# Optimization experiments

Measured on AMD Instinct MI355X. Metric: run time of the kernel, lower is better.

Reference implementation:

```python
import jax, jax.numpy as jnp
import numpy as np

EMBED_DIM = 512
NUM_HEADS = 8
HEAD_DIM = EMBED_DIM // NUM_HEADS
PAIR_BONUS = 2.0
MIN_SEPARATION = 3
PAIRING_MATRIX = jnp.array([
    [0, 1, 0, 0, 0],
    [1, 0, 1, 0, 0],
    [0, 1, 0, 1, 0],
    [0, 0, 1, 0, 0],
    [0, 0, 0, 0, 0],
], dtype=jnp.float32)


def setup_inputs() -> dict:
    key = jax.random.key(0)
    ks = jax.random.split(key, 12)
    B, S, E = 8, 1024, EMBED_DIM
    scale = 1.0 / np.sqrt(E)
    inp = {
        "query": jax.random.normal(ks[0], (B, S, E), dtype=jnp.float32),
        "key": jax.random.normal(ks[1], (B, S, E), dtype=jnp.float32),
        "value": jax.random.normal(ks[2], (B, S, E), dtype=jnp.float32),
        "nucleotide_sequence": jax.random.randint(ks[3], (B, S), 0, 5, dtype=jnp.int32),
        "key_padding_mask": jnp.zeros((B, S), dtype=bool),
        "Wq": jax.random.normal(ks[4], (E, E), dtype=jnp.float32) * scale,
        "bq": jnp.zeros((E,), dtype=jnp.float32),
        "Wk": jax.random.normal(ks[5], (E, E), dtype=jnp.float32) * scale,
        "bk": jnp.zeros((E,), dtype=jnp.float32),
        "Wv": jax.random.normal(ks[6], (E, E), dtype=jnp.float32) * scale,
        "bv": jnp.zeros((E,), dtype=jnp.float32),
        "Wo": jax.random.normal(ks[7], (E, E), dtype=jnp.float32) * scale,
        "bo": jnp.zeros((E,), dtype=jnp.float32),
    }
    return inp


def reference(query, key, value, nucleotide_sequence, key_padding_mask,
              Wq, bq, Wk, bk, Wv, bv, Wo, bo):
    B, T, E = query.shape
    S = key.shape[1]
    H, D = NUM_HEADS, HEAD_DIM
    scaling = D ** -0.5

    # projections -> (B, H, L, D)
    q = (query @ Wq + bq).reshape(B, T, H, D).transpose(0, 2, 1, 3)
    k = (key @ Wk + bk).reshape(B, S, H, D).transpose(0, 2, 1, 3)
    v = (value @ Wv + bv).reshape(B, S, H, D).transpose(0, 2, 1, 3)

    attn = jnp.einsum('bhtd,bhsd->bhts', q, k) * scaling  # (B,H,T,S)

    # base-pairing bias: gather into 5x5 table, masked by min separation
    pos = jnp.arange(S)
    sep_ok = (jnp.abs(pos[:, None] - pos[None, :]) >= MIN_SEPARATION).astype(jnp.float32)
    pairing = PAIRING_MATRIX[nucleotide_sequence[:, :, None], nucleotide_sequence[:, None, :]]  # (B,S,S)
    pair_bonus = pairing * sep_ok[None] * PAIR_BONUS
    attn = attn + pair_bonus[:, None, :, :]

    # key padding mask -> -inf
    attn = jnp.where(key_padding_mask[:, None, None, :], -jnp.inf, attn)

    attn_probs = jax.nn.softmax(attn, axis=-1)
    out = jnp.einsum('bhts,bhsd->bhtd', attn_probs, v)
    out = out.transpose(0, 2, 1, 3).reshape(B, T, E)
    out = out @ Wo + bo
    return out, attn_probs
```

## Files before the change

kernel.cpp:

```cpp
#include <hip/hip_runtime.h>
#include <hip/hip_bf16.h>
#include <stdint.h>


typedef float  f32x4  __attribute__((ext_vector_type(4)));
typedef short  s16x8  __attribute__((ext_vector_type(8)));

__device__ __forceinline__ ushort f2bf(float f) {
  union { float f; uint32_t u; } v; v.f = f;
  uint32_t u = v.u;
  return (ushort)((u + 0x7FFF + ((u >> 16) & 1)) >> 16);
}

__device__ __forceinline__ f32x4 mfma16(s16x8 a, s16x8 b, f32x4 c) {
  return __builtin_amdgcn_mfma_f32_16x16x32_bf16(a, b, c, 0, 0, 0);
}

__device__ __forceinline__ void gl_lds16(const void* g, void* l) {
  typedef __attribute__((address_space(1))) const void gvoid;
  typedef __attribute__((address_space(3))) void lvoid;
  __builtin_amdgcn_global_load_lds((gvoid*)(uintptr_t)g,
                                   (lvoid*)(uint32_t)(uintptr_t)l, 16, 0, 0);
}

__global__ __launch_bounds__(256) void k_convert_qkv(
    const float* __restrict__ q, const float* __restrict__ k,
    const float* __restrict__ v, ushort* __restrict__ Xbf) {
  size_t i = (size_t)blockIdx.x * 256 + threadIdx.x;
#pragma unroll
  for (int it = 0; it < 3; it++) {
    const float* src = (it == 0) ? q : (it == 1 ? k : v);
    float4 x = *reinterpret_cast<const float4*>(&src[i * 4]);
    uint2 o;
    o.x = (uint32_t)f2bf(x.x) | ((uint32_t)f2bf(x.y) << 16);
    o.y = (uint32_t)f2bf(x.z) | ((uint32_t)f2bf(x.w) << 16);
    *reinterpret_cast<uint2*>(&Xbf[((size_t)it * 1048576 + i) * 4]) = o;
  }
}

__global__ __launch_bounds__(256) void k_convert_w(
    const float* __restrict__ Wq, const float* __restrict__ Wk,
    const float* __restrict__ Wv, const float* __restrict__ Wo,
    ushort* __restrict__ WT, ushort* __restrict__ WoT) {
  int idx = blockIdx.x * 256 + threadIdx.x;
  int row = idx >> 9;
  int k = idx & 511;
  if (row < 1536) {
    const float* W = (row < 512) ? Wq : (row < 1024 ? Wk : Wv);
    int n = row & 511;
    WT[row * 512 + k] = f2bf(W[k * 512 + n]);
  } else {
    int n = row - 1536;
    WoT[n * 512 + k] = f2bf(Wo[k * 512 + n]);
  }
}

__global__ __launch_bounds__(256) void k_gemm_qkv(
    const ushort* __restrict__ Xbf, const ushort* __restrict__ WT,
    const float* __restrict__ bq, const float* __restrict__ bk,
    const float* __restrict__ bv, ushort* __restrict__ Y) {
  __shared__ ushort As[128 * 64];
  __shared__ ushort Bs[128 * 64];
  const int id = blockIdx.x;
  const int xcd = id & 7, slot = id >> 3;
  const int mb = xcd * 8 + slot / 12;
  const int nb = slot % 12;
  const int mat = nb >> 2;
  const float* bias = (mat == 0) ? bq : (mat == 1 ? bk : bv);
  const ushort* A = Xbf + (size_t)mat * 8192 * 512;
  const int tid = threadIdx.x;
  const int w = tid >> 6, l = tid & 63;
  const int wr = (w >> 1) * 64, wc = (w & 1) * 64;
  const int lr = l & 15, lg = l >> 4;
  const int srow = l >> 3, sslot = (l & 7) ^ srow;

  f32x4 acc[4][4];
#pragma unroll
  for (int i = 0; i < 4; i++)
#pragma unroll
    for (int j = 0; j < 4; j++) acc[i][j] = (f32x4){0.f, 0.f, 0.f, 0.f};

  for (int kk = 0; kk < 8; kk++) {
    const int k0 = kk * 64;
#pragma unroll
    for (int it = 0; it < 4; it++) {
      int g8 = it * 4 + w;
      int row = g8 * 8 + srow;
      gl_lds16(&A[(size_t)(mb * 128 + row) * 512 + k0 + sslot * 8], &As[g8 * 512]);
      gl_lds16(&WT[(size_t)(nb * 128 + row) * 512 + k0 + sslot * 8], &Bs[g8 * 512]);
    }
    __syncthreads();
#pragma unroll
    for (int ks = 0; ks < 2; ks++) {
      s16x8 af[4], bfr[4];
#pragma unroll
      for (int mt = 0; mt < 4; mt++) {
        int row = wr + mt * 16 + lr;
        af[mt] = *reinterpret_cast<const s16x8*>(
            (char*)As + row * 128 + ((ks * 64 + lg * 16) ^ ((row & 7) << 4)));
      }
#pragma unroll
      for (int nt = 0; nt < 4; nt++) {
        int row = wc + nt * 16 + lr;
        bfr[nt] = *reinterpret_cast<const s16x8*>(
            (char*)Bs + row * 128 + ((ks * 64 + lg * 16) ^ ((row & 7) << 4)));
      }
#pragma unroll
      for (int mt = 0; mt < 4; mt++)
#pragma unroll
        for (int nt = 0; nt < 4; nt++)
          acc[mt][nt] = mfma16(af[mt], bfr[nt], acc[mt][nt]);
    }
    __syncthreads();
  }
  const int ncb = nb * 128;
#pragma unroll
  for (int nt = 0; nt < 4; nt++) {
    int gcol = ncb + wc + nt * 16 + lr;
    float bv_ = bias[gcol & 511];
#pragma unroll
    for (int mt = 0; mt < 4; mt++) {
#pragma unroll
      for (int r = 0; r < 4; r++) {
        int grow = mb * 128 + wr + mt * 16 + lg * 4 + r;
        Y[(size_t)grow * 1536 + gcol] = f2bf(acc[mt][nt][r] + bv_);
      }
    }
  }
}

__global__ __launch_bounds__(256) void k_transpose_v(
    const ushort* __restrict__ Y, ushort* __restrict__ vT) {
  __shared__ ushort T[64 * 64];
  const int sc = blockIdx.x;
  const int bh = blockIdx.y;
  const int b = bh >> 3, h = bh & 7;
  const int s0 = sc * 64;
  const int tid = threadIdx.x;
#pragma unroll
  for (int it = 0; it < 2; it++) {
    int slot = it * 256 + tid;
    int srw = slot >> 3;
    int i16 = (slot & 7) * 16;
    int4 v = *reinterpret_cast<const int4*>(
        &Y[(size_t)(b * 1024 + s0 + srw) * 1536 + 1024 + h * 64 + (slot & 7) * 8]);
    *reinterpret_cast<int4*>((char*)T + srw * 128 + (i16 ^ ((srw & 7) << 4))) = v;
  }
  __syncthreads();
  const int d = tid >> 2;
  const int sseg = (tid & 3) * 16;
  int pk[8];
#pragma unroll
  for (int j = 0; j < 8; j++) {
    int s0l = sseg + 2 * j;
    uint32_t a = *reinterpret_cast<const ushort*>(
        (char*)T + s0l * 128 + ((d * 2) ^ ((s0l & 7) << 4)));
    uint32_t bb = *reinterpret_cast<const ushort*>(
        (char*)T + (s0l + 1) * 128 + ((d * 2) ^ (((s0l + 1) & 7) << 4)));
    pk[j] = (int)(a | (bb << 16));
  }
  ushort* dst = &vT[(size_t)(bh * 64 + d) * 1024 + s0 + sseg];
  int4 o0 = {pk[0], pk[1], pk[2], pk[3]};
  int4 o1 = {pk[4], pk[5], pk[6], pk[7]};
  *reinterpret_cast<int4*>(dst) = o0;
  *reinterpret_cast<int4*>(dst + 8) = o1;
}

__global__ __launch_bounds__(256) void k_attention(
    const ushort* __restrict__ Y, const ushort* __restrict__ vT,
    const int* __restrict__ seq, const unsigned char* __restrict__ mask,
    float* __restrict__ probs, ushort* __restrict__ AO) {
  __shared__ ushort Kb[2][64 * 64];
  __shared__ float Pb[16 * 68];
  __shared__ int seqm[1024];
  __shared__ float Rbuf[4 * 4 * 4 * 16];
  __shared__ float rinv_s[16];

  const int id = blockIdx.x;
  const int xcd = id & 7, slot = id >> 3;
  const int bh = xcd * 8 + (slot >> 6);
  const int tb = slot & 63;
  const int b = bh >> 3, h = bh & 7;
  const int tid = threadIdx.x;
  const int w = tid >> 6, l = tid & 63;
  const int lr = l & 15, lg = l >> 4;
  const int sc_ = w * 16;
  const int srow = l >> 3, sslot = (l & 7) ^ srow;

#pragma unroll
  for (int it = 0; it < 4; it++) {
    int s = it * 256 + tid;
    seqm[s] = seq[b * 1024 + s] | (mask[b * 1024 + s] ? 0x100 : 0);
  }
  const ushort* qp = &Y[(size_t)(b * 1024 + tb * 16 + lr) * 1536 + h * 64 + lg * 8];
  s16x8 qf0 = *reinterpret_cast<const s16x8*>(qp);
  s16x8 qf1 = *reinterpret_cast<const s16x8*>(qp + 32);

  f32x4 e[16];
  float psum[4] = {0.f, 0.f, 0.f, 0.f};

#pragma unroll
  for (int it = 0; it < 2; it++) {
    int g8 = it * 4 + w;
    int row = g8 * 8 + srow;
    gl_lds16(&Y[(size_t)(b * 1024 + row) * 1536 + 512 + h * 64 + sslot * 8],
             &Kb[0][g8 * 512]);
  }
  __syncthreads();

  int seqt[4];
#pragma unroll
  for (int r = 0; r < 4; r++) seqt[r] = seqm[tb * 16 + lg * 4 + r] & 255;

#pragma unroll
  for (int c = 0; c < 16; c++) {
    if (c < 15) {
#pragma unroll
      for (int it = 0; it < 2; it++) {
        int g8 = it * 4 + w;
        int row = (c + 1) * 64 + g8 * 8 + srow;
        gl_lds16(&Y[(size_t)(b * 1024 + row) * 1536 + 512 + h * 64 + sslot * 8],
                 &Kb[(c + 1) & 1][g8 * 512]);
      }
    }
    f32x4 facc = (f32x4){0.f, 0.f, 0.f, 0.f};
    const int srw = sc_ + lr;
#pragma unroll
    for (int ks = 0; ks < 2; ks++) {
      s16x8 kf = *reinterpret_cast<const s16x8*>(
          (char*)&Kb[c & 1][0] + srw * 128 + ((ks * 64 + lg * 16) ^ ((srw & 7) << 4)));
      facc = mfma16(ks == 0 ? qf0 : qf1, kf, facc);
    }
    const int sg = c * 64 + srw;
    const int sm = seqm[sg];
    const int ss = sm & 255;
    const bool msk = (sm & 0x100) != 0;
    f32x4 ev;
#pragma unroll
    for (int r = 0; r < 4; r++) {
      int tg = tb * 16 + lg * 4 + r;
      int dsep = tg - sg; dsep = dsep < 0 ? -dsep : dsep;
      int dnt = seqt[r] - ss; dnt = dnt < 0 ? -dnt : dnt;
      float bonus = (dnt == 1 && seqt[r] <= 3 && ss <= 3 && dsep >= 3) ? 2.0f : 0.0f;
      float v = facc[r] * 0.125f + bonus;
      float ee = msk ? 0.0f : __expf(v - 12.0f);
      ev[r] = ee;
      psum[r] += ee;
    }
    e[c] = ev;
    __syncthreads();
  }

#pragma unroll
  for (int r = 0; r < 4; r++) Rbuf[((w * 4 + lg) * 4 + r) * 16 + lr] = psum[r];
  __syncthreads();
  {
    int row = tid >> 4, j = tid & 15;
    int lgr = row >> 2, rr = row & 3;
    float s = 0.f;
#pragma unroll
    for (int i = 0; i < 4; i++) {
      int wj = j >> 2;
      int lrj = (j & 3) * 4 + i;
      s += Rbuf[((wj * 4 + lgr) * 4 + rr) * 16 + lrj];
    }
#pragma unroll
    for (int off = 1; off < 16; off <<= 1) s += __shfl_xor(s, off);
    if (j == 0) rinv_s[row] = 1.0f / s;
  }
  __syncthreads();
#pragma unroll
  for (int it = 0; it < 2; it++) {
    int g8 = it * 4 + w;
    int d = g8 * 8 + srow;
    gl_lds16(&vT[(size_t)(bh * 64 + d) * 1024 + sslot * 8], &Kb[0][g8 * 512]);
  }

  float rv[4];
#pragma unroll
  for (int r = 0; r < 4; r++) rv[r] = rinv_s[lg * 4 + r];
  const float rvp = rinv_s[tid >> 4];

  f32x4 oacc = (f32x4){0.f, 0.f, 0.f, 0.f};
#pragma unroll
  for (int c = 0; c < 16; c++) {
#pragma unroll
    for (int r = 0; r < 4; r++) Pb[(lg * 4 + r) * 68 + sc_ + lr] = e[c][r];
    __syncthreads();
    if (c < 15) {
#pragma unroll
      for (int it = 0; it < 2; it++) {
        int g8 = it * 4 + w;
        int d = g8 * 8 + srow;
        gl_lds16(&vT[(size_t)(bh * 64 + d) * 1024 + (c + 1) * 64 + sslot * 8],
                 &Kb[(c + 1) & 1][g8 * 512]);
      }
    }
#pragma unroll
    for (int ks = 0; ks < 2; ks++) {
      const float* pp = &Pb[lr * 68 + ks * 32 + lg * 8];
      float4 pa = *reinterpret_cast<const float4*>(pp);
      float4 pb = *reinterpret_cast<const float4*>(pp + 4);
      s16x8 paf = {(short)f2bf(pa.x), (short)f2bf(pa.y), (short)f2bf(pa.z),
                   (short)f2bf(pa.w), (short)f2bf(pb.x), (short)f2bf(pb.y),
                   (short)f2bf(pb.z), (short)f2bf(pb.w)};
      const int drow = sc_ + lr;
      s16x8 vb = *reinterpret_cast<const s16x8*>(
          (char*)&Kb[c & 1][0] + drow * 128 + ((ks * 64 + lg * 16) ^ ((drow & 7) << 4)));
      oacc = mfma16(paf, vb, oacc);
    }
    {
      int row = tid >> 4, j = tid & 15;
      float4 p4 = *reinterpret_cast<const float4*>(&Pb[row * 68 + j * 4]);
      float4 o;
      o.x = p4.x * rvp; o.y = p4.y * rvp; o.z = p4.z * rvp; o.w = p4.w * rvp;
      *reinterpret_cast<float4*>(
          &probs[((size_t)bh * 1024 + tb * 16 + row) * 1024 + c * 64 + j * 4]) = o;
    }
    __syncthreads();
  }
#pragma unroll
  for (int r = 0; r < 4; r++) {
    int t = tb * 16 + lg * 4 + r;
    AO[((size_t)b * 1024 + t) * 512 + h * 64 + sc_ + lr] = f2bf(oacc[r] * rv[r]);
  }
}

__global__ __launch_bounds__(256) void k_gemm_o(
    const ushort* __restrict__ AO, const ushort* __restrict__ WoT,
    const float* __restrict__ bo, float* __restrict__ out) {
  __shared__ ushort As[128 * 64];
  __shared__ ushort Bs[128 * 64];
  const int id = blockIdx.x;
  const int xcd = id & 7, slot = id >> 3;
  const int mb = xcd * 8 + (slot >> 2);
  const int nb = slot & 3;
  const int tid = threadIdx.x;
  const int w = tid >> 6, l = tid & 63;
  const int wr = (w >> 1) * 64, wc = (w & 1) * 64;
  const int lr = l & 15, lg = l >> 4;
  const int srow = l >> 3, sslot = (l & 7) ^ srow;

  f32x4 acc[4][4];
#pragma unroll
  for (int i = 0; i < 4; i++)
#pragma unroll
    for (int j = 0; j < 4; j++) acc[i][j] = (f32x4){0.f, 0.f, 0.f, 0.f};

  for (int kk = 0; kk < 8; kk++) {
    const int k0 = kk * 64;
#pragma unroll
    for (int it = 0; it < 4; it++) {
      int g8 = it * 4 + w;
      int row = g8 * 8 + srow;
      gl_lds16(&AO[(size_t)(mb * 128 + row) * 512 + k0 + sslot * 8], &As[g8 * 512]);
      gl_lds16(&WoT[(size_t)(nb * 128 + row) * 512 + k0 + sslot * 8], &Bs[g8 * 512]);
    }
    __syncthreads();
#pragma unroll
    for (int ks = 0; ks < 2; ks++) {
      s16x8 af[4], bfr[4];
#pragma unroll
      for (int mt = 0; mt < 4; mt++) {
        int row = wr + mt * 16 + lr;
        af[mt] = *reinterpret_cast<const s16x8*>(
            (char*)As + row * 128 + ((ks * 64 + lg * 16) ^ ((row & 7) << 4)));
      }
#pragma unroll
      for (int nt = 0; nt < 4; nt++) {
        int row = wc + nt * 16 + lr;
        bfr[nt] = *reinterpret_cast<const s16x8*>(
            (char*)Bs + row * 128 + ((ks * 64 + lg * 16) ^ ((row & 7) << 4)));
      }
#pragma unroll
      for (int mt = 0; mt < 4; mt++)
#pragma unroll
        for (int nt = 0; nt < 4; nt++)
          acc[mt][nt] = mfma16(af[mt], bfr[nt], acc[mt][nt]);
    }
    __syncthreads();
  }
  const int ncb = nb * 128;
#pragma unroll
  for (int nt = 0; nt < 4; nt++) {
    int gcol = ncb + wc + nt * 16 + lr;
    float bv_ = bo[gcol];
#pragma unroll
    for (int mt = 0; mt < 4; mt++) {
#pragma unroll
      for (int r = 0; r < 4; r++) {
        int grow = mb * 128 + wr + mt * 16 + lg * 4 + r;
        out[(size_t)grow * 512 + gcol] = acc[mt][nt][r] + bv_;
      }
    }
  }
}

extern "C" void kernel_launch(void* const* d_in, const int* in_sizes, int n_in,
                              void* d_out, int out_size, void* d_ws, size_t ws_size,
                              hipStream_t stream) {
  (void)in_sizes; (void)n_in; (void)out_size; (void)ws_size;
  const float* query = (const float*)d_in[0];
  const float* key   = (const float*)d_in[1];
  const float* value = (const float*)d_in[2];
  const int* seq     = (const int*)d_in[3];
  const unsigned char* mask = (const unsigned char*)d_in[4];
  const float* Wq = (const float*)d_in[5];
  const float* bq = (const float*)d_in[6];
  const float* Wk = (const float*)d_in[7];
  const float* bk = (const float*)d_in[8];
  const float* Wv = (const float*)d_in[9];
  const float* bv = (const float*)d_in[10];
  const float* Wo = (const float*)d_in[11];
  const float* bo = (const float*)d_in[12];

  float* out = (float*)d_out;
  float* probs = out + (size_t)8 * 1024 * 512;

  char* ws = (char*)d_ws;
  ushort* Y   = (ushort*)(ws);
  ushort* Xbf = (ushort*)(ws + 25165824);
  ushort* WT  = (ushort*)(ws + 50331648);
  ushort* WoT = (ushort*)(ws + 51904512);
  ushort* vT  = (ushort*)(ws + 25165824);
  ushort* AO  = (ushort*)(ws + 33554432);

  k_convert_qkv<<<4096, 256, 0, stream>>>(query, key, value, Xbf);
  k_convert_w<<<4096, 256, 0, stream>>>(Wq, Wk, Wv, Wo, WT, WoT);
  k_gemm_qkv<<<768, 256, 0, stream>>>(Xbf, WT, bq, bk, bv, Y);
  k_transpose_v<<<dim3(16, 64), 256, 0, stream>>>(Y, vT);
  k_attention<<<4096, 256, 0, stream>>>(Y, vT, seq, mask, probs, AO);
  k_gemm_o<<<256, 256, 0, stream>>>(AO, WoT, bo, out);
}
```

Baseline: 216.4 us.

## Fuse fp32-to-bf16 input conversion into QKV GEMM and recompute scores in attention

Removes the separate activation conversion kernel: the QKV GEMM now loads fp32 inputs, converts them to bf16 in registers and writes them into swizzled LDS. The attention kernel no longer keeps the 16 exp tiles in registers. It recomputes QK^T in a second pass, with the bonus and mask bits packed into bitmasks, and reads K and V fragments straight from global memory instead of staging them through LDS. It also sets a launch bound of 4 blocks per CU and writes bf16 probabilities to a smaller LDS tile. This trades register pressure and one kernel launch for doubled QK MFMA work, uncoalesced scalar stores of probs, and synchronous global loads in the GEMM.

```diff
diff --git a/kernel.cpp b/kernel.cpp
--- a/kernel.cpp
+++ b/kernel.cpp
@@ -21,21 +21,6 @@
   typedef __attribute__((address_space(3))) void lvoid;
   __builtin_amdgcn_global_load_lds((gvoid*)(uintptr_t)g,
                                    (lvoid*)(uint32_t)(uintptr_t)l, 16, 0, 0);
-}
-
-__global__ __launch_bounds__(256) void k_convert_qkv(
-    const float* __restrict__ q, const float* __restrict__ k,
-    const float* __restrict__ v, ushort* __restrict__ Xbf) {
-  size_t i = (size_t)blockIdx.x * 256 + threadIdx.x;
-#pragma unroll
-  for (int it = 0; it < 3; it++) {
-    const float* src = (it == 0) ? q : (it == 1 ? k : v);
-    float4 x = *reinterpret_cast<const float4*>(&src[i * 4]);
-    uint2 o;
-    o.x = (uint32_t)f2bf(x.x) | ((uint32_t)f2bf(x.y) << 16);
-    o.y = (uint32_t)f2bf(x.z) | ((uint32_t)f2bf(x.w) << 16);
-    *reinterpret_cast<uint2*>(&Xbf[((size_t)it * 1048576 + i) * 4]) = o;
-  }
 }
 
 __global__ __launch_bounds__(256) void k_convert_w(
@@ -56,7 +41,8 @@
 }
 
 __global__ __launch_bounds__(256) void k_gemm_qkv(
-    const ushort* __restrict__ Xbf, const ushort* __restrict__ WT,
+    const float* __restrict__ Aq, const float* __restrict__ Ak,
+    const float* __restrict__ Av, const ushort* __restrict__ WT,
     const float* __restrict__ bq, const float* __restrict__ bk,
     const float* __restrict__ bv, ushort* __restrict__ Y) {
   __shared__ ushort As[128 * 64];
@@ -66,8 +52,8 @@
   const int mb = xcd * 8 + slot / 12;
   const int nb = slot % 12;
   const int mat = nb >> 2;
+  const float* A    = (mat == 0) ? Aq : (mat == 1 ? Ak : Av);
   const float* bias = (mat == 0) ? bq : (mat == 1 ? bk : bv);
-  const ushort* A = Xbf + (size_t)mat * 8192 * 512;
   const int tid = threadIdx.x;
   const int w = tid >> 6, l = tid & 63;
   const int wr = (w >> 1) * 64, wc = (w & 1) * 64;
@@ -83,10 +69,21 @@
   for (int kk = 0; kk < 8; kk++) {
     const int k0 = kk * 64;
 #pragma unroll
+    for (int it = 0; it < 8; it++) {
+      int s2 = it * 256 + tid;
+      int row = s2 >> 4;
+      int k4 = (s2 & 15) * 4;
+      float4 v = *reinterpret_cast<const float4*>(
+          &A[(size_t)(mb * 128 + row) * 512 + k0 + k4]);
+      uint64_t p = (uint64_t)f2bf(v.x) | ((uint64_t)f2bf(v.y) << 16) |
+                   ((uint64_t)f2bf(v.z) << 32) | ((uint64_t)f2bf(v.w) << 48);
+      int boff = row * 128 + ((k4 * 2) ^ ((row & 7) << 4));
+      *reinterpret_cast<uint64_t*>((char*)As + boff) = p;
+    }
+#pragma unroll
     for (int it = 0; it < 4; it++) {
       int g8 = it * 4 + w;
       int row = g8 * 8 + srow;
-      gl_lds16(&A[(size_t)(mb * 128 + row) * 512 + k0 + sslot * 8], &As[g8 * 512]);
       gl_lds16(&WT[(size_t)(nb * 128 + row) * 512 + k0 + sslot * 8], &Bs[g8 * 512]);
     }
     __syncthreads();
@@ -166,14 +163,13 @@
   *reinterpret_cast<int4*>(dst + 8) = o1;
 }
 
-__global__ __launch_bounds__(256) void k_attention(
+__global__ __launch_bounds__(256, 4) void k_attention(
     const ushort* __restrict__ Y, const ushort* __restrict__ vT,
     const int* __restrict__ seq, const unsigned char* __restrict__ mask,
     float* __restrict__ probs, ushort* __restrict__ AO) {
-  __shared__ ushort Kb[2][64 * 64];
-  __shared__ float Pb[16 * 68];
   __shared__ int seqm[1024];
-  __shared__ float Rbuf[4 * 4 * 4 * 16];
+  __shared__ ushort Pb[16 * 72];
+  __shared__ float Rbuf[1024];
   __shared__ float rinv_s[16];
 
   const int id = blockIdx.x;
@@ -185,7 +181,6 @@
   const int w = tid >> 6, l = tid & 63;
   const int lr = l & 15, lg = l >> 4;
   const int sc_ = w * 16;
-  const int srow = l >> 3, sslot = (l & 7) ^ srow;
 
 #pragma unroll
   for (int it = 0; it < 4; it++) {
@@ -195,60 +190,43 @@
   const ushort* qp = &Y[(size_t)(b * 1024 + tb * 16 + lr) * 1536 + h * 64 + lg * 8];
   s16x8 qf0 = *reinterpret_cast<const s16x8*>(qp);
   s16x8 qf1 = *reinterpret_cast<const s16x8*>(qp + 32);
-
-  f32x4 e[16];
+  __syncthreads();
+
+  int seqt[4];
+#pragma unroll
+  for (int r = 0; r < 4; r++) seqt[r] = seqm[tb * 16 + lg * 4 + r] & 255;
+
+  const ushort* kbase = &Y[(size_t)(b * 1024) * 1536 + 512 + h * 64];
+  const int srw = sc_ + lr;
+
+  uint32_t bb0 = 0, bb1 = 0, mk = 0;
   float psum[4] = {0.f, 0.f, 0.f, 0.f};
-
-#pragma unroll
-  for (int it = 0; it < 2; it++) {
-    int g8 = it * 4 + w;
-    int row = g8 * 8 + srow;
-    gl_lds16(&Y[(size_t)(b * 1024 + row) * 1536 + 512 + h * 64 + sslot * 8],
-             &Kb[0][g8 * 512]);
-  }
-  __syncthreads();
-
-  int seqt[4];
-#pragma unroll
-  for (int r = 0; r < 4; r++) seqt[r] = seqm[tb * 16 + lg * 4 + r] & 255;
-
 #pragma unroll
   for (int c = 0; c < 16; c++) {
-    if (c < 15) {
-#pragma unroll
-      for (int it = 0; it < 2; it++) {
-        int g8 = it * 4 + w;
-        int row = (c + 1) * 64 + g8 * 8 + srow;
-        gl_lds16(&Y[(size_t)(b * 1024 + row) * 1536 + 512 + h * 64 + sslot * 8],
-                 &Kb[(c + 1) & 1][g8 * 512]);
-      }
-    }
+    const int sg = c * 64 + srw;
+    const ushort* kp = kbase + (size_t)sg * 1536;
+    s16x8 kf0 = *reinterpret_cast<const s16x8*>(kp + lg * 8);
+    s16x8 kf1 = *reinterpret_cast<const s16x8*>(kp + 32 + lg * 8);
     f32x4 facc = (f32x4){0.f, 0.f, 0.f, 0.f};
-    const int srw = sc_ + lr;
-#pragma unroll
-    for (int ks = 0; ks < 2; ks++) {
-      s16x8 kf = *reinterpret_cast<const s16x8*>(
-          (char*)&Kb[c & 1][0] + srw * 128 + ((ks * 64 + lg * 16) ^ ((srw & 7) << 4)));
-      facc = mfma16(ks == 0 ? qf0 : qf1, kf, facc);
-    }
-    const int sg = c * 64 + srw;
+    facc = mfma16(qf0, kf0, facc);
+    facc = mfma16(qf1, kf1, facc);
     const int sm = seqm[sg];
     const int ss = sm & 255;
     const bool msk = (sm & 0x100) != 0;
-    f32x4 ev;
+    uint32_t bits = 0;
 #pragma unroll
     for (int r = 0; r < 4; r++) {
       int tg = tb * 16 + lg * 4 + r;
       int dsep = tg - sg; dsep = dsep < 0 ? -dsep : dsep;
       int dnt = seqt[r] - ss; dnt = dnt < 0 ? -dnt : dnt;
-      float bonus = (dnt == 1 && seqt[r] <= 3 && ss <= 3 && dsep >= 3) ? 2.0f : 0.0f;
-      float v = facc[r] * 0.125f + bonus;
+      bool bon = (dnt == 1 && seqt[r] <= 3 && ss <= 3 && dsep >= 3);
+      float v = facc[r] * 0.125f + (bon ? 2.0f : 0.0f);
       float ee = msk ? 0.0f : __expf(v - 12.0f);
-      ev[r] = ee;
       psum[r] += ee;
-    }
-    e[c] = ev;
-    __syncthreads();
+      bits |= (bon ? 1u : 0u) << r;
+    }
+    if (c < 8) bb0 |= bits << (4 * c); else bb1 |= bits << (4 * (c - 8));
+    mk |= (msk ? 1u : 0u) << c;
   }
 
 #pragma unroll
@@ -269,53 +247,38 @@
     if (j == 0) rinv_s[row] = 1.0f / s;
   }
   __syncthreads();
-#pragma unroll
-  for (int it = 0; it < 2; it++) {
-    int g8 = it * 4 + w;
-    int d = g8 * 8 + srow;
-    gl_lds16(&vT[(size_t)(bh * 64 + d) * 1024 + sslot * 8], &Kb[0][g8 * 512]);
-  }
-
   float rv[4];
 #pragma unroll
   for (int r = 0; r < 4; r++) rv[r] = rinv_s[lg * 4 + r];
-  const float rvp = rinv_s[tid >> 4];
 
   f32x4 oacc = (f32x4){0.f, 0.f, 0.f, 0.f};
+  const ushort* vbase = &vT[(size_t)(bh * 64) * 1024];
 #pragma unroll
   for (int c = 0; c < 16; c++) {
-#pragma unroll
-    for (int r = 0; r < 4; r++) Pb[(lg * 4 + r) * 68 + sc_ + lr] = e[c][r];
-    __syncthreads();
-    if (c < 15) {
-#pragma unroll
-      for (int it = 0; it < 2; it++) {
-        int g8 = it * 4 + w;
-        int d = g8 * 8 + srow;
-        gl_lds16(&vT[(size_t)(bh * 64 + d) * 1024 + (c + 1) * 64 + sslot * 8],
-                 &Kb[(c + 1) & 1][g8 * 512]);
-      }
-    }
+    const int sg = c * 64 + srw;
+    const ushort* kp = kbase + (size_t)sg * 1536;
+    s16x8 kf0 = *reinterpret_cast<const s16x8*>(kp + lg * 8);
+    s16x8 kf1 = *reinterpret_cast<const s16x8*>(kp + 32 + lg * 8);
+    f32x4 facc = (f32x4){0.f, 0.f, 0.f, 0.f};
+    facc = mfma16(qf0, kf0, facc);
+    facc = mfma16(qf1, kf1, facc);
+    const uint32_t bits = ((c < 8) ? (bb0 >> (4 * c)) : (bb1 >> (4 * (c - 8)))) & 15u;
+    const bool msk = (mk >> c) & 1u;
+#pragma unroll
+    for (int r = 0; r < 4; r++) {
+      float v = facc[r] * 0.125f + (((bits >> r) & 1u) ? 2.0f : 0.0f);
+      float ee = msk ? 0.0f : __expf(v - 12.0f);
+      probs[((size_t)bh * 1024 + tb * 16 + lg * 4 + r) * 1024 + c * 64 + srw] =
+          ee * rv[r];
+      Pb[(lg * 4 + r) * 72 + srw] = f2bf(ee);
+    }
+    __syncthreads();
 #pragma unroll
     for (int ks = 0; ks < 2; ks++) {
-      const float* pp = &Pb[lr * 68 + ks * 32 + lg * 8];
-      float4 pa = *reinterpret_cast<const float4*>(pp);
-      float4 pb = *reinterpret_cast<const float4*>(pp + 4);
-      s16x8 paf = {(short)f2bf(pa.x), (short)f2bf(pa.y), (short)f2bf(pa.z),
-                   (short)f2bf(pa.w), (short)f2bf(pb.x), (short)f2bf(pb.y),
-                   (short)f2bf(pb.z), (short)f2bf(pb.w)};
-      const int drow = sc_ + lr;
+      s16x8 paf = *reinterpret_cast<const s16x8*>(&Pb[lr * 72 + ks * 32 + lg * 8]);
       s16x8 vb = *reinterpret_cast<const s16x8*>(
-          (char*)&Kb[c & 1][0] + drow * 128 + ((ks * 64 + lg * 16) ^ ((drow & 7) << 4)));
+          &vbase[(size_t)(sc_ + lr) * 1024 + c * 64 + ks * 32 + lg * 8]);
       oacc = mfma16(paf, vb, oacc);
-    }
-    {
-      int row = tid >> 4, j = tid & 15;
-      float4 p4 = *reinterpret_cast<const float4*>(&Pb[row * 68 + j * 4]);
-      float4 o;
-      o.x = p4.x * rvp; o.y = p4.y * rvp; o.z = p4.z * rvp; o.w = p4.w * rvp;
-      *reinterpret_cast<float4*>(
-          &probs[((size_t)bh * 1024 + tb * 16 + row) * 1024 + c * 64 + j * 4]) = o;
     }
     __syncthreads();
   }
@@ -419,15 +382,13 @@
 
   char* ws = (char*)d_ws;
   ushort* Y   = (ushort*)(ws);
-  ushort* Xbf = (ushort*)(ws + 25165824);
-  ushort* WT  = (ushort*)(ws + 50331648);
-  ushort* WoT = (ushort*)(ws + 51904512);
-  ushort* vT  = (ushort*)(ws + 25165824);
-  ushort* AO  = (ushort*)(ws + 33554432);
-
-  k_convert_qkv<<<4096, 256, 0, stream>>>(query, key, value, Xbf);
+  ushort* WT  = (ushort*)(ws + 25165824);
+  ushort* WoT = (ushort*)(ws + 26738688);
+  ushort* vT  = (ushort*)(ws + 27262976);
+  ushort* AO  = (ushort*)(ws + 35651584);
+
   k_convert_w<<<4096, 256, 0, stream>>>(Wq, Wk, Wv, Wo, WT, WoT);
-  k_gemm_qkv<<<768, 256, 0, stream>>>(Xbf, WT, bq, bk, bv, Y);
+  k_gemm_qkv<<<768, 256, 0, stream>>>(query, key, value, WT, bq, bk, bv, Y);
   k_transpose_v<<<dim3(16, 64), 256, 0, stream>>>(Y, vT);
   k_attention<<<4096, 256, 0, stream>>>(Y, vT, seq, mask, probs, AO);
   k_gemm_o<<<256, 256, 0, stream>>>(AO, WoT, bo, out);
```

Result: slower. 275.0 us (+27.1%).
